# Kernel optimization log

Hardware: AMD Instinct MI355X
Metric: run time of the kernel (lower is better)

Reference implementation:

```python
import jax, jax.numpy as jnp
import numpy as np

B, S, QD, KD, AD, H = 64, 2048, 1024, 512, 512, 8
NEG = -1e10  # masked_fill value from original code
SCALING = 1.0  # default forward arg


def setup_inputs() -> dict:
    key = jax.random.key(0)
    ks = jax.random.split(key, 6)
    query = jax.random.normal(ks[0], (B, QD), dtype=jnp.float32)
    keys = jax.random.normal(ks[1], (B, S, KD), dtype=jnp.float32)
    value = jax.random.normal(ks[2], (B, S, KD), dtype=jnp.float32)
    key_len = jax.random.randint(ks[3], (B,), 1, S + 1, dtype=jnp.int32)
    Wq = jax.random.normal(ks[4], (H, AD, QD), dtype=jnp.float32) * 0.02
    Wk = jax.random.normal(ks[5], (H, AD, KD), dtype=jnp.float32) * 0.02
    return {"query": query, "keys": keys, "value": value, "key_len": key_len,
            "Wq": Wq, "Wk": Wk}


def reference(query, keys, value, key_len, Wq, Wk):
    # per-head query projection: (B, H, AD)
    q = jnp.einsum('bq,haq->bha', query, Wq)
    # per-head key projection: (B, H, S, AD)
    k = jnp.einsum('bsk,hak->bhsa', keys, Wk)
    # single-step dot attention energies: (B, H, S)
    energy = jnp.einsum('bha,bhsa->bhs', q, k)
    # padding mask: positions >= key_len are masked
    mask = jnp.arange(keys.shape[1])[None, None, :] >= key_len[:, None, None]
    energy = jnp.where(mask, NEG, energy)
    attn = jax.nn.softmax(energy * SCALING, axis=-1)  # (B, H, S)
    # per-head contexts: (B, H, KD), concatenated over heads -> (B, H*KD)
    context = jnp.einsum('bhs,bsd->bhd', attn, value)
    contexts = context.reshape(context.shape[0], -1)
    return contexts, attn
```

## Files before the change

kernel.cpp:

```cpp
#include <hip/hip_runtime.h>
#include <math.h>


#define B_  64
#define S_  2048
#define QD_ 1024
#define KD_ 512
#define AD_ 512
#define H_  8

__global__ __launch_bounds__(256) void k1_qproj(const float* __restrict__ query,
                                                const float* __restrict__ Wq,
                                                float* __restrict__ qo) {
    __shared__ float As[16][65];
    __shared__ float Ws[64][65];
    const int t = threadIdx.x;
    const int m0 = blockIdx.x * 16, n0 = blockIdx.y * 64;
    const int nl = t & 63, mb = (t >> 6) * 4;
    float acc[4] = {0.f, 0.f, 0.f, 0.f};
    for (int kc = 0; kc < QD_; kc += 64) {
#pragma unroll
        for (int i = 0; i < 4; ++i) {
            int idx = t + i * 256, r = idx >> 6, c = idx & 63;
            As[r][c] = query[(m0 + r) * QD_ + kc + c];
        }
#pragma unroll
        for (int i = 0; i < 16; ++i) {
            int idx = t + i * 256, r = idx >> 6, c = idx & 63;
            Ws[r][c] = Wq[(size_t)(n0 + r) * QD_ + kc + c];
        }
        __syncthreads();
#pragma unroll
        for (int k = 0; k < 64; ++k) {
            float w = Ws[nl][k];
#pragma unroll
            for (int j = 0; j < 4; ++j) acc[j] += As[mb + j][k] * w;
        }
        __syncthreads();
    }
#pragma unroll
    for (int j = 0; j < 4; ++j)
        qo[(m0 + mb + j) * (H_ * AD_) + n0 + nl] = acc[j];
}

__global__ __launch_bounds__(256) void k2_qk(const float* __restrict__ q,
                                             const float* __restrict__ Wk,
                                             float* __restrict__ qk) {
    __shared__ float As[16][65];
    __shared__ float Ws[64][65];
    const int t = threadIdx.x;
    const int m0 = blockIdx.x * 16, n0 = blockIdx.y * 64, h = blockIdx.z;
    const float* Wh = Wk + (size_t)h * AD_ * KD_;
    const int nl = t & 63, mb = (t >> 6) * 4;
    float acc[4] = {0.f, 0.f, 0.f, 0.f};
    for (int ac = 0; ac < AD_; ac += 64) {
#pragma unroll
        for (int i = 0; i < 4; ++i) {
            int idx = t + i * 256, r = idx >> 6, c = idx & 63;
            As[r][c] = q[(m0 + r) * (H_ * AD_) + h * AD_ + ac + c];
        }
#pragma unroll
        for (int i = 0; i < 16; ++i) {
            int idx = t + i * 256, r = idx >> 6, c = idx & 63;
            Ws[r][c] = Wh[(size_t)(ac + r) * KD_ + n0 + c];
        }
        __syncthreads();
#pragma unroll
        for (int k = 0; k < 64; ++k) {
            float w = Ws[k][nl];
#pragma unroll
            for (int j = 0; j < 4; ++j) acc[j] += As[mb + j][k] * w;
        }
        __syncthreads();
    }
#pragma unroll
    for (int j = 0; j < 4; ++j)
        qk[(m0 + mb + j) * (H_ * KD_) + h * KD_ + n0 + nl] = acc[j];
}

__global__ __launch_bounds__(256) void k3_energy(const float* __restrict__ keys,
                                                 const float* __restrict__ qk,
                                                 const int* __restrict__ key_len,
                                                 float* __restrict__ energy) {
    const int b = blockIdx.y;
    const int klen = key_len[b];
    const int s0 = blockIdx.x * 64;
    if (s0 >= klen) return;
    const int t = threadIdx.x;
    const int lane = t & 63, w = t >> 6;

    const float4* qk4 = reinterpret_cast<const float4*>(qk + (size_t)b * (H_ * KD_));
    float qkr[8][8];
#pragma unroll
    for (int h = 0; h < H_; ++h) {
        float4 u0 = qk4[h * (KD_ / 4) + lane * 2];
        float4 u1 = qk4[h * (KD_ / 4) + lane * 2 + 1];
        qkr[h][0] = u0.x; qkr[h][1] = u0.y; qkr[h][2] = u0.z; qkr[h][3] = u0.w;
        qkr[h][4] = u1.x; qkr[h][5] = u1.y; qkr[h][6] = u1.z; qkr[h][7] = u1.w;
    }

    const int sbeg = s0 + w * 16;
    const int count = min(16, klen - sbeg);
    if (count <= 0) return;

    auto row = [&](int s) {
        const float4* kp = reinterpret_cast<const float4*>(
            keys + (size_t)(b * S_ + s) * KD_ + lane * 8);
        float4 k0 = kp[0], k1 = kp[1];
        float kf[8] = {k0.x, k0.y, k0.z, k0.w, k1.x, k1.y, k1.z, k1.w};
        float p[8];
#pragma unroll
        for (int h = 0; h < 8; ++h) {
            float a = 0.f;
#pragma unroll
            for (int j = 0; j < 8; ++j) a += kf[j] * qkr[h][j];
            p[h] = a;
        }
#pragma unroll
        for (int j = 0; j < 4; ++j) {
            float keep = (lane & 1) ? p[j + 4] : p[j];
            float send = (lane & 1) ? p[j] : p[j + 4];
            p[j] = keep + __shfl_xor(send, 1, 64);
        }
#pragma unroll
        for (int j = 0; j < 2; ++j) {
            float keep = (lane & 2) ? p[j + 2] : p[j];
            float send = (lane & 2) ? p[j] : p[j + 2];
            p[j] = keep + __shfl_xor(send, 2, 64);
        }
        {
            float keep = (lane & 4) ? p[1] : p[0];
            float send = (lane & 4) ? p[0] : p[1];
            p[0] = keep + __shfl_xor(send, 4, 64);
        }
        p[0] += __shfl_xor(p[0], 8, 64);
        p[0] += __shfl_xor(p[0], 16, 64);
        p[0] += __shfl_xor(p[0], 32, 64);
        if (lane < 8) {
            const int h = ((lane & 1) << 2) | (lane & 2) | ((lane >> 2) & 1);
            energy[((size_t)b * H_ + h) * S_ + s] = p[0];
        }
    };

    if (count == 16) {
#pragma unroll 4
        for (int i = 0; i < 16; ++i) row(sbeg + i);
    } else {
        for (int i = 0; i < count; ++i) row(sbeg + i);
    }
}

__global__ __launch_bounds__(256) void k4_softmax(const float* __restrict__ energy,
                                                  const int* __restrict__ key_len,
                                                  float* __restrict__ attn) {
    const int bh = blockIdx.x;
    const int b = bh >> 3;
    const int t = threadIdx.x;

    const int klen = key_len[b];
    const float* e = energy + (size_t)bh * S_;
    float ev[8];
    float m = -3.0e38f;
#pragma unroll
    for (int j = 0; j < 8; ++j) {
        int s = t + j * 256;
        float x = (s < klen) ? e[s] : -3.0e38f;
        ev[j] = x;
        m = fmaxf(m, x);
    }
#pragma unroll
    for (int off = 32; off >= 1; off >>= 1) m = fmaxf(m, __shfl_xor(m, off, 64));
    __shared__ float redm[4];
    if ((t & 63) == 0) redm[t >> 6] = m;
    __syncthreads();
    m = fmaxf(fmaxf(redm[0], redm[1]), fmaxf(redm[2], redm[3]));

    float sum = 0.f;
#pragma unroll
    for (int j = 0; j < 8; ++j) {
        int s = t + j * 256;
        float p = (s < klen) ? __expf(ev[j] - m) : 0.f;
        ev[j] = p;
        sum += p;
    }
#pragma unroll
    for (int off = 32; off >= 1; off >>= 1) sum += __shfl_xor(sum, off, 64);
    __shared__ float reds[4];
    if ((t & 63) == 0) reds[t >> 6] = sum;
    __syncthreads();
    sum = reds[0] + reds[1] + reds[2] + reds[3];
    const float inv = 1.f / sum;

    float* a = attn + (size_t)bh * S_;
#pragma unroll
    for (int j = 0; j < 8; ++j) a[t + j * 256] = ev[j] * inv;
}

__global__ __launch_bounds__(256) void k5_context(const float* __restrict__ value,
                                                  const float* __restrict__ attn,
                                                  const int* __restrict__ key_len,
                                                  float* __restrict__ part) {
    const int b = blockIdx.y;
    const int klen = key_len[b];
    const int s_base = blockIdx.x * 128;
    if (s_base >= klen) return;
    const int t = threadIdx.x;

    __shared__ float at[8][128];
#pragma unroll
    for (int i = 0; i < 4; ++i) {
        int idx = t + i * 256, h = idx >> 7, si = idx & 127;
        int s = s_base + si;
        at[h][si] = (s < klen) ? attn[((size_t)b * H_ + h) * S_ + s] : 0.f;
    }
    __syncthreads();

    const int col = t & 127;
    const int sh = t >> 7;
    const int d = col * 4;
    const int base_si = sh * 64;
    const int valid = min(64, klen - s_base - base_si);
    if (valid <= 0) return;

    float4 acc[8];
#pragma unroll
    for (int h = 0; h < H_; ++h) acc[h] = make_float4(0.f, 0.f, 0.f, 0.f);

    auto step = [&](int si) {
        const float4 v = *reinterpret_cast<const float4*>(
            value + (size_t)(b * S_ + s_base + base_si + si) * KD_ + d);
#pragma unroll
        for (int h = 0; h < H_; ++h) {
            const float a = at[h][base_si + si];
            acc[h].x += a * v.x; acc[h].y += a * v.y;
            acc[h].z += a * v.z; acc[h].w += a * v.w;
        }
    };
    if (valid == 64) {
#pragma unroll 4
        for (int si = 0; si < 64; ++si) step(si);
    } else {
        for (int si = 0; si < valid; ++si) step(si);
    }

    const int p = blockIdx.x * 2 + sh;
    float* pp = part + (((size_t)p * B_ + b) * H_) * KD_;
#pragma unroll
    for (int h = 0; h < H_; ++h)
        *reinterpret_cast<float4*>(pp + h * KD_ + d) = acc[h];
}

__global__ __launch_bounds__(256) void k6_reduce(const float* __restrict__ part,
                                                 const int* __restrict__ key_len,
                                                 float* __restrict__ ctx) {
    const int g = blockIdx.x * 256 + threadIdx.x;
    const int d4 = g & 127;
    const int h = (g >> 7) & 7;
    const int b = g >> 10;
    const int nc = (key_len[b] + 63) >> 6;
    float4 s = make_float4(0.f, 0.f, 0.f, 0.f);
    for (int p = 0; p < nc; ++p) {
        const float4 v = *reinterpret_cast<const float4*>(
            part + (((size_t)p * B_ + b) * H_ + h) * KD_ + d4 * 4);
        s.x += v.x; s.y += v.y; s.z += v.z; s.w += v.w;
    }
    *reinterpret_cast<float4*>(ctx + ((size_t)b * H_ + h) * KD_ + d4 * 4) = s;
}

extern "C" void kernel_launch(void* const* d_in, const int* in_sizes, int n_in,
                              void* d_out, int out_size, void* d_ws, size_t ws_size,
                              hipStream_t stream) {
    const float* query   = (const float*)d_in[0];
    const float* keys    = (const float*)d_in[1];
    const float* value   = (const float*)d_in[2];
    const int*   key_len = (const int*)d_in[3];
    const float* Wq      = (const float*)d_in[4];
    const float* Wk      = (const float*)d_in[5];

    float* out = (float*)d_out;
    float* ctx_out  = out;
    float* attn_out = out + (size_t)B_ * H_ * KD_;

    float* ws      = (float*)d_ws;
    float* q_ws    = ws;
    float* qk_ws   = ws + (size_t)B_ * H_ * AD_;
    float* e_ws    = qk_ws + (size_t)B_ * H_ * KD_;
    float* part_ws = e_ws + (size_t)B_ * H_ * S_;

    hipLaunchKernelGGL(k1_qproj, dim3(4, 64), dim3(256), 0, stream, query, Wq, q_ws);
    hipLaunchKernelGGL(k2_qk, dim3(4, 8, 8), dim3(256), 0, stream, q_ws, Wk, qk_ws);
    hipLaunchKernelGGL(k3_energy, dim3(32, 64), dim3(256), 0, stream,
                       keys, qk_ws, key_len, e_ws);
    hipLaunchKernelGGL(k4_softmax, dim3(512), dim3(256), 0, stream,
                       e_ws, key_len, attn_out);
    hipLaunchKernelGGL(k5_context, dim3(16, 64), dim3(256), 0, stream,
                       value, attn_out, key_len, part_ws);
    hipLaunchKernelGGL(k6_reduce, dim3(256), dim3(256), 0, stream,
                       part_ws, key_len, ctx_out);
}
```

Baseline: 585.2 us.

## Transpose qk layout and compute energies one key row per thread

k2 now writes the projected query-key vectors in a [b][kd][h] layout. k3_energy then gives each thread one whole key row, accumulating all 8 heads with wave-uniform reads of qkT, so the cross-lane shuffle reduction goes away. The catch is that each lane now strides through its own 2 KB row instead of lanes sharing coalesced row reads, which can hurt memory efficiency on the largest input. Separately, k5_context now processes 256 positions per block instead of 128, which halves the partial sums that k6 has to reduce.

```diff
diff --git a/kernel.cpp b/kernel.cpp
--- a/kernel.cpp
+++ b/kernel.cpp
@@ -45,7 +45,7 @@
 
 __global__ __launch_bounds__(256) void k2_qk(const float* __restrict__ q,
                                              const float* __restrict__ Wk,
-                                             float* __restrict__ qk) {
+                                             float* __restrict__ qkT) {
     __shared__ float As[16][65];
     __shared__ float Ws[64][65];
     const int t = threadIdx.x;
@@ -75,78 +75,46 @@
     }
 #pragma unroll
     for (int j = 0; j < 4; ++j)
-        qk[(m0 + mb + j) * (H_ * KD_) + h * KD_ + n0 + nl] = acc[j];
-}
-
-__global__ __launch_bounds__(256) void k3_energy(const float* __restrict__ keys,
-                                                 const float* __restrict__ qk,
+        qkT[((size_t)(m0 + mb + j) * KD_ + (n0 + nl)) * H_ + h] = acc[j];
+}
+
+__global__ __launch_bounds__(128) void k3_energy(const float* __restrict__ keys,
+                                                 const float* __restrict__ qkT,
                                                  const int* __restrict__ key_len,
                                                  float* __restrict__ energy) {
     const int b = blockIdx.y;
     const int klen = key_len[b];
-    const int s0 = blockIdx.x * 64;
-    if (s0 >= klen) return;
-    const int t = threadIdx.x;
-    const int lane = t & 63, w = t >> 6;
-
-    const float4* qk4 = reinterpret_cast<const float4*>(qk + (size_t)b * (H_ * KD_));
-    float qkr[8][8];
-#pragma unroll
-    for (int h = 0; h < H_; ++h) {
-        float4 u0 = qk4[h * (KD_ / 4) + lane * 2];
-        float4 u1 = qk4[h * (KD_ / 4) + lane * 2 + 1];
-        qkr[h][0] = u0.x; qkr[h][1] = u0.y; qkr[h][2] = u0.z; qkr[h][3] = u0.w;
-        qkr[h][4] = u1.x; qkr[h][5] = u1.y; qkr[h][6] = u1.z; qkr[h][7] = u1.w;
-    }
-
-    const int sbeg = s0 + w * 16;
-    const int count = min(16, klen - sbeg);
-    if (count <= 0) return;
-
-    auto row = [&](int s) {
-        const float4* kp = reinterpret_cast<const float4*>(
-            keys + (size_t)(b * S_ + s) * KD_ + lane * 8);
-        float4 k0 = kp[0], k1 = kp[1];
-        float kf[8] = {k0.x, k0.y, k0.z, k0.w, k1.x, k1.y, k1.z, k1.w};
-        float p[8];
-#pragma unroll
-        for (int h = 0; h < 8; ++h) {
-            float a = 0.f;
-#pragma unroll
-            for (int j = 0; j < 8; ++j) a += kf[j] * qkr[h][j];
-            p[h] = a;
-        }
-#pragma unroll
-        for (int j = 0; j < 4; ++j) {
-            float keep = (lane & 1) ? p[j + 4] : p[j];
-            float send = (lane & 1) ? p[j] : p[j + 4];
-            p[j] = keep + __shfl_xor(send, 1, 64);
-        }
-#pragma unroll
-        for (int j = 0; j < 2; ++j) {
-            float keep = (lane & 2) ? p[j + 2] : p[j];
-            float send = (lane & 2) ? p[j] : p[j + 2];
-            p[j] = keep + __shfl_xor(send, 2, 64);
-        }
-        {
-            float keep = (lane & 4) ? p[1] : p[0];
-            float send = (lane & 4) ? p[0] : p[1];
-            p[0] = keep + __shfl_xor(send, 4, 64);
-        }
-        p[0] += __shfl_xor(p[0], 8, 64);
-        p[0] += __shfl_xor(p[0], 16, 64);
-        p[0] += __shfl_xor(p[0], 32, 64);
-        if (lane < 8) {
-            const int h = ((lane & 1) << 2) | (lane & 2) | ((lane >> 2) & 1);
-            energy[((size_t)b * H_ + h) * S_ + s] = p[0];
-        }
-    };
-
-    if (count == 16) {
-#pragma unroll 4
-        for (int i = 0; i < 16; ++i) row(sbeg + i);
-    } else {
-        for (int i = 0; i < count; ++i) row(sbeg + i);
+    const int s_base = blockIdx.x * 128;
+    if (s_base >= klen) return;
+    const int t = threadIdx.x;
+    const int row = s_base + t;
+
+    const float* __restrict__ qb = qkT + (size_t)b * (KD_ * H_);
+    const float4* __restrict__ kr =
+        reinterpret_cast<const float4*>(keys + (size_t)(b * S_ + row) * KD_);
+
+    float acc[8];
+#pragma unroll
+    for (int h = 0; h < H_; ++h) acc[h] = 0.f;
+
+#pragma unroll 2
+    for (int j4 = 0; j4 < KD_ / 4; ++j4) {
+        const float4 kv = kr[j4];
+        const float* qd = qb + (size_t)j4 * 4 * H_;
+#pragma unroll
+        for (int h = 0; h < H_; ++h) acc[h] += kv.x * qd[h];
+#pragma unroll
+        for (int h = 0; h < H_; ++h) acc[h] += kv.y * qd[H_ + h];
+#pragma unroll
+        for (int h = 0; h < H_; ++h) acc[h] += kv.z * qd[2 * H_ + h];
+#pragma unroll
+        for (int h = 0; h < H_; ++h) acc[h] += kv.w * qd[3 * H_ + h];
+    }
+
+    if (row < klen) {
+#pragma unroll
+        for (int h = 0; h < H_; ++h)
+            energy[((size_t)b * H_ + h) * S_ + row] = acc[h];
     }
 }
 
@@ -202,14 +170,14 @@
                                                   float* __restrict__ part) {
     const int b = blockIdx.y;
     const int klen = key_len[b];
-    const int s_base = blockIdx.x * 128;
+    const int s_base = blockIdx.x * 256;
     if (s_base >= klen) return;
     const int t = threadIdx.x;
 
-    __shared__ float at[8][128];
-#pragma unroll
-    for (int i = 0; i < 4; ++i) {
-        int idx = t + i * 256, h = idx >> 7, si = idx & 127;
+    __shared__ float at[8][256];
+#pragma unroll
+    for (int i = 0; i < 8; ++i) {
+        int idx = t + i * 256, h = idx >> 8, si = idx & 255;
         int s = s_base + si;
         at[h][si] = (s < klen) ? attn[((size_t)b * H_ + h) * S_ + s] : 0.f;
     }
@@ -218,8 +186,8 @@
     const int col = t & 127;
     const int sh = t >> 7;
     const int d = col * 4;
-    const int base_si = sh * 64;
-    const int valid = min(64, klen - s_base - base_si);
+    const int base_si = sh * 128;
+    const int valid = min(128, klen - s_base - base_si);
     if (valid <= 0) return;
 
     float4 acc[8];
@@ -236,9 +204,9 @@
             acc[h].z += a * v.z; acc[h].w += a * v.w;
         }
     };
-    if (valid == 64) {
+    if (valid == 128) {
 #pragma unroll 4
-        for (int si = 0; si < 64; ++si) step(si);
+        for (int si = 0; si < 128; ++si) step(si);
     } else {
         for (int si = 0; si < valid; ++si) step(si);
     }
@@ -257,7 +225,7 @@
     const int d4 = g & 127;
     const int h = (g >> 7) & 7;
     const int b = g >> 10;
-    const int nc = (key_len[b] + 63) >> 6;
+    const int nc = (key_len[b] + 127) >> 7;
     float4 s = make_float4(0.f, 0.f, 0.f, 0.f);
     for (int p = 0; p < nc; ++p) {
         const float4 v = *reinterpret_cast<const float4*>(
@@ -283,17 +251,17 @@
 
     float* ws      = (float*)d_ws;
     float* q_ws    = ws;
-    float* qk_ws   = ws + (size_t)B_ * H_ * AD_;
-    float* e_ws    = qk_ws + (size_t)B_ * H_ * KD_;
+    float* qkT_ws  = ws + (size_t)B_ * H_ * AD_;
+    float* e_ws    = qkT_ws + (size_t)B_ * KD_ * H_;
     float* part_ws = e_ws + (size_t)B_ * H_ * S_;
 
     hipLaunchKernelGGL(k1_qproj, dim3(4, 64), dim3(256), 0, stream, query, Wq, q_ws);
-    hipLaunchKernelGGL(k2_qk, dim3(4, 8, 8), dim3(256), 0, stream, q_ws, Wk, qk_ws);
-    hipLaunchKernelGGL(k3_energy, dim3(32, 64), dim3(256), 0, stream,
-                       keys, qk_ws, key_len, e_ws);
+    hipLaunchKernelGGL(k2_qk, dim3(4, 8, 8), dim3(256), 0, stream, q_ws, Wk, qkT_ws);
+    hipLaunchKernelGGL(k3_energy, dim3(16, 64), dim3(128), 0, stream,
+                       keys, qkT_ws, key_len, e_ws);
     hipLaunchKernelGGL(k4_softmax, dim3(512), dim3(256), 0, stream,
                        e_ws, key_len, attn_out);
-    hipLaunchKernelGGL(k5_context, dim3(16, 64), dim3(256), 0, stream,
+    hipLaunchKernelGGL(k5_context, dim3(8, 64), dim3(256), 0, stream,
                        value, attn_out, key_len, part_ws);
     hipLaunchKernelGGL(k6_reduce, dim3(256), dim3(256), 0, stream,
                        part_ws, key_len, ctx_out);
```

Result: no change. 588.3 us (+0.5%).
